# Performance work log

Hardware: AMD Instinct MI355X
Metric: run time of the kernel (lower is better)

The kernel has to match this reference:

```python
import jax, jax.numpy as jnp
import numpy as np

B, T, D, H = 32, 1024, 512, 512


def setup_inputs() -> dict:
    key = jax.random.key(0)
    ks = jax.random.split(key, 9)
    K = 1.0 / np.sqrt(H)
    u = lambda k, s: jax.random.uniform(k, s, jnp.float32, -K, K)
    return {
        "x": jax.random.normal(ks[0], (B, T, D), jnp.float32),
        "w_ih_fw": u(ks[1], (3 * H, D)),
        "w_hh_fw": u(ks[2], (3 * H, H)),
        "b_ih_fw": u(ks[3], (3 * H,)),
        "b_hh_fw": u(ks[4], (3 * H,)),
        "w_ih_bw": u(ks[5], (3 * H, D)),
        "w_hh_bw": u(ks[6], (3 * H, H)),
        "b_ih_bw": u(ks[7], (3 * H,)),
        "b_hh_bw": u(ks[8], (3 * H,)),
    }


def _gru_scan(x, w_ih, w_hh, b_ih, b_hh, reverse):
    # x: (B, T, D) -> precompute input projections for all steps: (T, B, 3H)
    b, t, d = x.shape
    h_dim = w_hh.shape[1]
    ih = jnp.einsum("btd,gd->tbg", x, w_ih) + b_ih

    def step(h, ih_t):
        hh = h @ w_hh.T + b_hh  # (B, 3H)
        r = jax.nn.sigmoid(ih_t[:, :h_dim] + hh[:, :h_dim])
        z = jax.nn.sigmoid(ih_t[:, h_dim:2 * h_dim] + hh[:, h_dim:2 * h_dim])
        n = jnp.tanh(ih_t[:, 2 * h_dim:] + r * hh[:, 2 * h_dim:])
        h_new = (1.0 - z) * n + z * h
        return h_new, h_new

    h0 = jnp.zeros((b, h_dim), x.dtype)
    h_last, ys = jax.lax.scan(step, h0, ih, reverse=reverse)
    # ys: (T, B, H), aligned to original time indices even when reverse=True
    return jnp.transpose(ys, (1, 0, 2)), h_last


def reference(x, w_ih_fw, w_hh_fw, b_ih_fw, b_hh_fw, w_ih_bw, w_hh_bw, b_ih_bw, b_hh_bw):
    out_fw, h_fw = _gru_scan(x, w_ih_fw, w_hh_fw, b_ih_fw, b_hh_fw, reverse=False)
    out_bw, h_bw = _gru_scan(x, w_ih_bw, w_hh_bw, b_ih_bw, b_hh_bw, reverse=True)
    outputs = jnp.concatenate([out_fw, out_bw], axis=-1)  # (B, T, 2H)
    return outputs, h_fw, h_bw
```

## Files before the change

kernel.cpp:

```cpp
#include <hip/hip_runtime.h>


#define T_LEN 1024
#define B_SZ  32
#define D_SZ  512
#define H_SZ  512
#define NWG_DIR 32
#define JW 16
#define NTHR 512

typedef __attribute__((ext_vector_type(8))) _Float16 half8;
typedef __attribute__((ext_vector_type(4))) float f32x4;
typedef __attribute__((ext_vector_type(4))) int int4v;

__device__ __forceinline__ _Float16 f2h(float f) { return (_Float16)f; }
__device__ __forceinline__ float sigm_f(float v) {
  return __builtin_amdgcn_rcpf(1.f + __expf(-v));
}
__device__ __forceinline__ float tanh_f(float v) {
  return 1.f - 2.f * __builtin_amdgcn_rcpf(1.f + __expf(2.f * v));
}
__device__ __forceinline__ void bar_lgkm() {
  asm volatile("s_waitcnt lgkmcnt(0)\ns_barrier" ::: "memory");
}

__global__ __launch_bounds__(NTHR, 2)
void gru2_persistent(const float* __restrict__ x,
                     const float* __restrict__ wih_fw, const float* __restrict__ whh_fw,
                     const float* __restrict__ bih_fw, const float* __restrict__ bhh_fw,
                     const float* __restrict__ wih_bw, const float* __restrict__ whh_bw,
                     const float* __restrict__ bih_bw, const float* __restrict__ bhh_bw,
                     float* __restrict__ out,
                     unsigned* __restrict__ hexu,
                     unsigned* __restrict__ flags)
{
  __shared__ float Cp[24 * 272];
  __shared__ float biasLds[96];

  const int bid  = blockIdx.x;
  const int dir  = bid >> 5;
  const int g    = bid & 31;
  const int tid  = threadIdx.x;
  const int wave = tid >> 6;
  const int lane = tid & 63;

  const float* wih = dir ? wih_bw : wih_fw;
  const float* whh = dir ? whh_bw : whh_fw;
  const float* bih = dir ? bih_bw : bih_fw;
  const float* bhh = dir ? bhh_bw : bhh_fw;

  if (tid < 48) {
    int grow = (tid >> 4) * H_SZ + g * JW + (tid & 15);
    biasLds[tid]      = bih[grow];
    biasLds[48 + tid] = bhh[grow];
  }

  const bool isHh = (wave >= 4);
  const int  wv   = wave & 3;
  const int  wm   = wv & 1;
  const int  kh   = wv >> 1;

  half8 Bf[3][8];
  {
    const float* W = isHh ? whh : wih;
    #pragma unroll
    for (int gam = 0; gam < 3; ++gam) {
      const int row = gam * H_SZ + g * JW + (lane & 15);
      #pragma unroll
      for (int i = 0; i < 8; ++i) {
        const float* src = W + (size_t)row * D_SZ + (kh * 8 + i) * 32 + ((lane >> 4) << 3);
        float4 v0 = *(const float4*)(src);
        float4 v1 = *(const float4*)(src + 4);
        half8 b;
        b[0]=f2h(v0.x); b[1]=f2h(v0.y); b[2]=f2h(v0.z); b[3]=f2h(v0.w);
        b[4]=f2h(v1.x); b[5]=f2h(v1.y); b[6]=f2h(v1.z); b[7]=f2h(v1.w);
        Bf[gam][i] = b;
      }
    }
  }

  const int arow = wm * 16 + (lane & 15);
  const int koff = (lane >> 4) << 3;
  const float* const xwavebase = x + (size_t)arow * T_LEN * D_SZ + kh * 256 + koff;

  float4 xn[16];
  if (!isHh) {
    const int t0 = dir ? (T_LEN - 1) : 0;
    const float* base = xwavebase + (size_t)t0 * D_SZ;
    #pragma unroll
    for (int i = 0; i < 8; ++i) {
      xn[2*i]   = *(const float4*)(base + i * 32);
      xn[2*i+1] = *(const float4*)(base + i * 32 + 4);
    }
  }
  __syncthreads();

  float hreg = 0.f;
  const int gb = tid >> 4;
  const int gj = tid & 15;
  float* hlast = out + (size_t)B_SZ * T_LEN * (2 * H_SZ) + (size_t)dir * B_SZ * H_SZ;
  const unsigned* const fa = flags + (size_t)dir * NWG_DIR + kh * 16 + (lane & 15);

  for (int s = 0; s < T_LEN; ++s) {
    const int t = dir ? (T_LEN - 1 - s) : s;
    const bool hasNext = (s + 1 < T_LEN);

    f32x4 acc[3] = {{0.f,0.f,0.f,0.f},{0.f,0.f,0.f,0.f},{0.f,0.f,0.f,0.f}};

    if (!isHh) {
      half8 a[8];
      #pragma unroll
      for (int i = 0; i < 8; ++i) {
        float4 u = xn[2*i], w = xn[2*i+1];
        half8 h;
        h[0]=f2h(u.x); h[1]=f2h(u.y); h[2]=f2h(u.z); h[3]=f2h(u.w);
        h[4]=f2h(w.x); h[5]=f2h(w.y); h[6]=f2h(w.z); h[7]=f2h(w.w);
        a[i] = h;
      }
      #pragma unroll
      for (int i = 0; i < 8; ++i)
        #pragma unroll
        for (int gam = 0; gam < 3; ++gam)
          acc[gam] = __builtin_amdgcn_mfma_f32_16x16x32_f16(a[i], Bf[gam][i], acc[gam], 0, 0, 0);
    } else if (s > 0) {
      {
        unsigned va, vb;
        asm volatile("global_load_dword %0, %1, off sc0 sc1" : "=&v"(va) : "v"(fa));
        asm volatile("global_load_dword %0, %1, off sc0 sc1" : "=&v"(vb) : "v"(fa));
        for (;;) {
          asm volatile("s_waitcnt vmcnt(1)" ::: "memory");
          if (__all(va >= (unsigned)s)) break;
          asm volatile("global_load_dword %0, %1, off sc0 sc1" : "=&v"(va) : "v"(fa));
          asm volatile("s_waitcnt vmcnt(1)" ::: "memory");
          if (__all(vb >= (unsigned)s)) break;
          asm volatile("global_load_dword %0, %1, off sc0 sc1" : "=&v"(vb) : "v"(fa));
        }
        asm volatile("s_waitcnt vmcnt(0)" ::: "memory");
      }
      const char* p0 = (const char*)hexu
          + (((size_t)dir * 2 + ((s - 1) & 1)) * (B_SZ * (H_SZ / 2))) * 4
          + (size_t)arow * (H_SZ * 2) + (size_t)(kh * 256 + koff) * 2;
      int4v hv[8];
      asm volatile(
        "global_load_dwordx4 %0, %8, off sc0 sc1\n\t"
        "global_load_dwordx4 %1, %8, off offset:64 sc0 sc1\n\t"
        "global_load_dwordx4 %2, %8, off offset:128 sc0 sc1\n\t"
        "global_load_dwordx4 %3, %8, off offset:192 sc0 sc1\n\t"
        "global_load_dwordx4 %4, %8, off offset:256 sc0 sc1\n\t"
        "global_load_dwordx4 %5, %8, off offset:320 sc0 sc1\n\t"
        "global_load_dwordx4 %6, %8, off offset:384 sc0 sc1\n\t"
        "global_load_dwordx4 %7, %8, off offset:448 sc0 sc1\n\t"
        "s_waitcnt vmcnt(0)"
        : "=&v"(hv[0]), "=&v"(hv[1]), "=&v"(hv[2]), "=&v"(hv[3]),
          "=&v"(hv[4]), "=&v"(hv[5]), "=&v"(hv[6]), "=&v"(hv[7])
        : "v"(p0) : "memory");
      __builtin_amdgcn_sched_barrier(0);
      #pragma unroll
      for (int i = 0; i < 8; ++i) {
        half8 a = __builtin_bit_cast(half8, hv[i]);
        #pragma unroll
        for (int gam = 0; gam < 3; ++gam)
          acc[gam] = __builtin_amdgcn_mfma_f32_16x16x32_f16(a, Bf[gam][i], acc[gam], 0, 0, 0);
      }
    }

    {
      const int src = isHh ? 1 : 0;
      #pragma unroll
      for (int gam = 0; gam < 3; ++gam) {
        float* cp = Cp + (size_t)(((src*2 + kh)*3 + gam)*2 + wm) * 272
                       + ((lane >> 4) << 2) * 17 + (lane & 15);
        #pragma unroll
        for (int vv2 = 0; vv2 < 4; ++vv2) cp[vv2 * 17] = acc[gam][vv2];
      }
    }
    bar_lgkm();

    float hnS;
    {
      const int mb = gb >> 4, rb = gb & 15;
      float sih[3], shh[3];
      #pragma unroll
      for (int gam = 0; gam < 3; ++gam) {
        float aih = 0.f, ahh = 0.f;
        #pragma unroll
        for (int q = 0; q < 2; ++q) {
          aih += Cp[(size_t)(((0*2+q)*3+gam)*2 + mb) * 272 + rb * 17 + gj];
          ahh += Cp[(size_t)(((1*2+q)*3+gam)*2 + mb) * 272 + rb * 17 + gj];
        }
        sih[gam] = aih + biasLds[gam * 16 + gj];
        shh[gam] = ahh + biasLds[48 + gam * 16 + gj];
      }
      const float r = sigm_f(sih[0] + shh[0]);
      const float z = sigm_f(sih[1] + shh[1]);
      const float n = tanh_f(sih[2] + r * shh[2]);
      const float hn = (1.f - z) * n + z * hreg;
      hreg = hn;
      hnS = hn;

      const float hother = __shfl_xor(hn, 1);
      if ((gj & 1) == 0) {
        union { unsigned u; _Float16 h[2]; } pr;
        pr.h[0] = f2h(hn); pr.h[1] = f2h(hother);
        unsigned* hp = hexu + ((size_t)dir * 2 + (s & 1)) * (B_SZ * (H_SZ / 2))
                     + (size_t)gb * (H_SZ / 2) + (g * JW + gj) / 2;
        __hip_atomic_store(hp, pr.u, __ATOMIC_RELAXED, __HIP_MEMORY_SCOPE_AGENT);
      }
    }
    asm volatile("s_waitcnt vmcnt(0)" ::: "memory");
    bar_lgkm();
    if (tid == 0)
      __hip_atomic_store((unsigned*)&flags[(size_t)dir * NWG_DIR + g],
                         (unsigned)(s + 1),
                         __ATOMIC_RELAXED, __HIP_MEMORY_SCOPE_AGENT);

    out[((size_t)gb * T_LEN + t) * (2 * H_SZ) + dir * H_SZ + g * JW + gj] = hnS;
    if (s == T_LEN - 1) hlast[gb * H_SZ + g * JW + gj] = hnS;
    if (!isHh && hasNext) {
      const int tn = dir ? (T_LEN - 2 - s) : (s + 1);
      const float* base = xwavebase + (size_t)tn * D_SZ;
      #pragma unroll
      for (int i = 0; i < 8; ++i) {
        xn[2*i]   = *(const float4*)(base + i * 32);
        xn[2*i+1] = *(const float4*)(base + i * 32 + 4);
      }
    }
  }
}

extern "C" void kernel_launch(void* const* d_in, const int* in_sizes, int n_in,
                              void* d_out, int out_size, void* d_ws, size_t ws_size,
                              hipStream_t stream) {
  const float* x      = (const float*)d_in[0];
  const float* wih_fw = (const float*)d_in[1];
  const float* whh_fw = (const float*)d_in[2];
  const float* bih_fw = (const float*)d_in[3];
  const float* bhh_fw = (const float*)d_in[4];
  const float* wih_bw = (const float*)d_in[5];
  const float* whh_bw = (const float*)d_in[6];
  const float* bih_bw = (const float*)d_in[7];
  const float* bhh_bw = (const float*)d_in[8];
  float* out = (float*)d_out;

  const size_t FLAGS_BYTES = 256;
  const size_t HEX_BYTES   = (size_t)2 * 2 * B_SZ * (H_SZ / 2) * sizeof(unsigned);
  if (ws_size < FLAGS_BYTES + HEX_BYTES) return;

  unsigned* flags = (unsigned*)d_ws;
  unsigned* hexu  = (unsigned*)((char*)d_ws + FLAGS_BYTES);

  hipMemsetAsync(flags, 0, FLAGS_BYTES, stream);
  gru2_persistent<<<dim3(64), dim3(NTHR), 0, stream>>>(
      x, wih_fw, whh_fw, bih_fw, bhh_fw, wih_bw, whh_bw, bih_bw, bhh_bw,
      out, hexu, flags);
}
```

Measured before the change: 4.414 ms.

## Co-locate each direction's workgroups on one XCD and use XCD-local coherence for exchange

The launch grows to 256 workgroups and keeps only those with blockIdx%8 in {0,1}, relying on round-robin XCD dispatch so each direction's 32 workgroups share one XCD. At startup every workgroup records its XCC id and checks that each direction is uniform and the two directions differ. If so, hidden-state exchange and flag polling use sc0-only loads and stores, which go through the shared L2 instead of bypassing to device-coherent memory. A grid-wide spin barrier and fallback paths guard against other placements, at the cost of extra startup synchronisation, more code, and reliance on undocumented dispatch order.

```diff
diff --git a/kernel.cpp b/kernel.cpp
--- a/kernel.cpp
+++ b/kernel.cpp
@@ -32,14 +32,19 @@
                      const float* __restrict__ bih_bw, const float* __restrict__ bhh_bw,
                      float* __restrict__ out,
                      unsigned* __restrict__ hexu,
-                     unsigned* __restrict__ flags)
+                     unsigned* __restrict__ flags,
+                     unsigned* __restrict__ xcdmap,
+                     unsigned* __restrict__ gbar)
 {
+  const int bid = blockIdx.x;
+  const int dir = bid & 7;
+  if (dir >= 2) return;
+  const int g = bid >> 3;
+
   __shared__ float Cp[24 * 272];
   __shared__ float biasLds[96];
-
-  const int bid  = blockIdx.x;
-  const int dir  = bid >> 5;
-  const int g    = bid & 31;
+  __shared__ int fastSh;
+
   const int tid  = threadIdx.x;
   const int wave = tid >> 6;
   const int lane = tid & 63;
@@ -54,6 +59,43 @@
     biasLds[tid]      = bih[grow];
     biasLds[48 + tid] = bhh[grow];
   }
+
+  {
+    unsigned xcc;
+    asm volatile("s_getreg_b32 %0, hwreg(20, 0, 32)" : "=s"(xcc));
+    if (tid == 0)
+      __hip_atomic_store(&xcdmap[dir * NWG_DIR + g], xcc + 1u,
+                         __ATOMIC_RELAXED, __HIP_MEMORY_SCOPE_AGENT);
+    if (wave == 0) {
+      unsigned v = 0u; int bud = 1 << 16; bool ok = true;
+      for (;;) {
+        v = __hip_atomic_load(&xcdmap[lane], __ATOMIC_RELAXED,
+                              __HIP_MEMORY_SCOPE_AGENT);
+        if (__all(v != 0u)) break;
+        if (--bud < 0) { ok = false; break; }
+        __builtin_amdgcn_s_sleep(8);
+      }
+      const unsigned ref0 = __shfl(v, 0);
+      const unsigned ref1 = __shfl(v, NWG_DIR);
+      const bool uni = __all((lane < NWG_DIR) ? (v == ref0) : (v == ref1));
+      if (lane == 0) fastSh = (ok && uni && ref0 != ref1) ? 1 : 0;
+    }
+  }
+  __syncthreads();
+  const bool fast = (fastSh != 0);
+  __builtin_amdgcn_fence(__ATOMIC_ACQUIRE, "agent");
+  __syncthreads();
+
+  if (tid == 0) {
+    __hip_atomic_fetch_add(gbar, 1u, __ATOMIC_RELAXED, __HIP_MEMORY_SCOPE_AGENT);
+    int bud = 1 << 20;
+    while (__hip_atomic_load(gbar, __ATOMIC_RELAXED,
+                             __HIP_MEMORY_SCOPE_AGENT) < 64u) {
+      if (--bud < 0) break;
+      __builtin_amdgcn_s_sleep(8);
+    }
+  }
+  __syncthreads();
 
   const bool isHh = (wave >= 4);
   const int  wv   = wave & 3;
@@ -100,6 +142,7 @@
   const int gj = tid & 15;
   float* hlast = out + (size_t)B_SZ * T_LEN * (2 * H_SZ) + (size_t)dir * B_SZ * H_SZ;
   const unsigned* const fa = flags + (size_t)dir * NWG_DIR + kh * 16 + (lane & 15);
+  int pollbud = 1 << 21;
 
   for (int s = 0; s < T_LEN; ++s) {
     const int t = dir ? (T_LEN - 1 - s) : s;
@@ -123,44 +166,79 @@
         for (int gam = 0; gam < 3; ++gam)
           acc[gam] = __builtin_amdgcn_mfma_f32_16x16x32_f16(a[i], Bf[gam][i], acc[gam], 0, 0, 0);
     } else if (s > 0) {
-      {
-        unsigned va, vb;
-        asm volatile("global_load_dword %0, %1, off sc0 sc1" : "=&v"(va) : "v"(fa));
-        asm volatile("global_load_dword %0, %1, off sc0 sc1" : "=&v"(vb) : "v"(fa));
+      if (fast) {
         for (;;) {
-          asm volatile("s_waitcnt vmcnt(1)" ::: "memory");
-          if (__all(va >= (unsigned)s)) break;
+          unsigned vv;
+          asm volatile("global_load_dword %0, %1, off sc0\ns_waitcnt vmcnt(0)"
+                       : "=&v"(vv) : "v"(fa) : "memory");
+          if (__all(vv >= (unsigned)s)) break;
+          if (--pollbud < 0) break;
+        }
+        const char* p0 = (const char*)hexu
+            + (((size_t)dir * 2 + ((s - 1) & 1)) * (B_SZ * (H_SZ / 2))) * 4
+            + (size_t)arow * (H_SZ * 2) + (size_t)(kh * 256 + koff) * 2;
+        int4v hv[8];
+        asm volatile(
+          "global_load_dwordx4 %0, %8, off sc0\n\t"
+          "global_load_dwordx4 %1, %8, off offset:64 sc0\n\t"
+          "global_load_dwordx4 %2, %8, off offset:128 sc0\n\t"
+          "global_load_dwordx4 %3, %8, off offset:192 sc0\n\t"
+          "global_load_dwordx4 %4, %8, off offset:256 sc0\n\t"
+          "global_load_dwordx4 %5, %8, off offset:320 sc0\n\t"
+          "global_load_dwordx4 %6, %8, off offset:384 sc0\n\t"
+          "global_load_dwordx4 %7, %8, off offset:448 sc0\n\t"
+          "s_waitcnt vmcnt(0)"
+          : "=&v"(hv[0]), "=&v"(hv[1]), "=&v"(hv[2]), "=&v"(hv[3]),
+            "=&v"(hv[4]), "=&v"(hv[5]), "=&v"(hv[6]), "=&v"(hv[7])
+          : "v"(p0) : "memory");
+        __builtin_amdgcn_sched_barrier(0);
+        #pragma unroll
+        for (int i = 0; i < 8; ++i) {
+          half8 a = __builtin_bit_cast(half8, hv[i]);
+          #pragma unroll
+          for (int gam = 0; gam < 3; ++gam)
+            acc[gam] = __builtin_amdgcn_mfma_f32_16x16x32_f16(a, Bf[gam][i], acc[gam], 0, 0, 0);
+        }
+      } else {
+        {
+          unsigned va, vb;
           asm volatile("global_load_dword %0, %1, off sc0 sc1" : "=&v"(va) : "v"(fa));
-          asm volatile("s_waitcnt vmcnt(1)" ::: "memory");
-          if (__all(vb >= (unsigned)s)) break;
           asm volatile("global_load_dword %0, %1, off sc0 sc1" : "=&v"(vb) : "v"(fa));
-        }
-        asm volatile("s_waitcnt vmcnt(0)" ::: "memory");
-      }
-      const char* p0 = (const char*)hexu
-          + (((size_t)dir * 2 + ((s - 1) & 1)) * (B_SZ * (H_SZ / 2))) * 4
-          + (size_t)arow * (H_SZ * 2) + (size_t)(kh * 256 + koff) * 2;
-      int4v hv[8];
-      asm volatile(
-        "global_load_dwordx4 %0, %8, off sc0 sc1\n\t"
-        "global_load_dwordx4 %1, %8, off offset:64 sc0 sc1\n\t"
-        "global_load_dwordx4 %2, %8, off offset:128 sc0 sc1\n\t"
-        "global_load_dwordx4 %3, %8, off offset:192 sc0 sc1\n\t"
-        "global_load_dwordx4 %4, %8, off offset:256 sc0 sc1\n\t"
-        "global_load_dwordx4 %5, %8, off offset:320 sc0 sc1\n\t"
-        "global_load_dwordx4 %6, %8, off offset:384 sc0 sc1\n\t"
-        "global_load_dwordx4 %7, %8, off offset:448 sc0 sc1\n\t"
-        "s_waitcnt vmcnt(0)"
-        : "=&v"(hv[0]), "=&v"(hv[1]), "=&v"(hv[2]), "=&v"(hv[3]),
-          "=&v"(hv[4]), "=&v"(hv[5]), "=&v"(hv[6]), "=&v"(hv[7])
-        : "v"(p0) : "memory");
-      __builtin_amdgcn_sched_barrier(0);
-      #pragma unroll
-      for (int i = 0; i < 8; ++i) {
-        half8 a = __builtin_bit_cast(half8, hv[i]);
-        #pragma unroll
-        for (int gam = 0; gam < 3; ++gam)
-          acc[gam] = __builtin_amdgcn_mfma_f32_16x16x32_f16(a, Bf[gam][i], acc[gam], 0, 0, 0);
+          for (;;) {
+            asm volatile("s_waitcnt vmcnt(1)" ::: "memory");
+            if (__all(va >= (unsigned)s)) break;
+            asm volatile("global_load_dword %0, %1, off sc0 sc1" : "=&v"(va) : "v"(fa));
+            asm volatile("s_waitcnt vmcnt(1)" ::: "memory");
+            if (__all(vb >= (unsigned)s)) break;
+            asm volatile("global_load_dword %0, %1, off sc0 sc1" : "=&v"(vb) : "v"(fa));
+          }
+          asm volatile("s_waitcnt vmcnt(0)" ::: "memory");
+        }
+        const char* p0 = (const char*)hexu
+            + (((size_t)dir * 2 + ((s - 1) & 1)) * (B_SZ * (H_SZ / 2))) * 4
+            + (size_t)arow * (H_SZ * 2) + (size_t)(kh * 256 + koff) * 2;
+        int4v hv[8];
+        asm volatile(
+          "global_load_dwordx4 %0, %8, off sc0 sc1\n\t"
+          "global_load_dwordx4 %1, %8, off offset:64 sc0 sc1\n\t"
+          "global_load_dwordx4 %2, %8, off offset:128 sc0 sc1\n\t"
+          "global_load_dwordx4 %3, %8, off offset:192 sc0 sc1\n\t"
+          "global_load_dwordx4 %4, %8, off offset:256 sc0 sc1\n\t"
+          "global_load_dwordx4 %5, %8, off offset:320 sc0 sc1\n\t"
+          "global_load_dwordx4 %6, %8, off offset:384 sc0 sc1\n\t"
+          "global_load_dwordx4 %7, %8, off offset:448 sc0 sc1\n\t"
+          "s_waitcnt vmcnt(0)"
+          : "=&v"(hv[0]), "=&v"(hv[1]), "=&v"(hv[2]), "=&v"(hv[3]),
+            "=&v"(hv[4]), "=&v"(hv[5]), "=&v"(hv[6]), "=&v"(hv[7])
+          : "v"(p0) : "memory");
+        __builtin_amdgcn_sched_barrier(0);
+        #pragma unroll
+        for (int i = 0; i < 8; ++i) {
+          half8 a = __builtin_bit_cast(half8, hv[i]);
+          #pragma unroll
+          for (int gam = 0; gam < 3; ++gam)
+            acc[gam] = __builtin_amdgcn_mfma_f32_16x16x32_f16(a, Bf[gam][i], acc[gam], 0, 0, 0);
+        }
       }
     }
 
@@ -204,15 +282,24 @@
         pr.h[0] = f2h(hn); pr.h[1] = f2h(hother);
         unsigned* hp = hexu + ((size_t)dir * 2 + (s & 1)) * (B_SZ * (H_SZ / 2))
                      + (size_t)gb * (H_SZ / 2) + (g * JW + gj) / 2;
-        __hip_atomic_store(hp, pr.u, __ATOMIC_RELAXED, __HIP_MEMORY_SCOPE_AGENT);
+        if (fast)
+          asm volatile("global_store_dword %0, %1, off sc0"
+                       :: "v"(hp), "v"(pr.u) : "memory");
+        else
+          __hip_atomic_store(hp, pr.u, __ATOMIC_RELAXED, __HIP_MEMORY_SCOPE_AGENT);
       }
     }
     asm volatile("s_waitcnt vmcnt(0)" ::: "memory");
     bar_lgkm();
-    if (tid == 0)
-      __hip_atomic_store((unsigned*)&flags[(size_t)dir * NWG_DIR + g],
-                         (unsigned)(s + 1),
-                         __ATOMIC_RELAXED, __HIP_MEMORY_SCOPE_AGENT);
+    if (tid == 0) {
+      unsigned* fp = flags + (size_t)dir * NWG_DIR + g;
+      const unsigned fv = (unsigned)(s + 1);
+      if (fast)
+        asm volatile("global_store_dword %0, %1, off sc0"
+                     :: "v"(fp), "v"(fv) : "memory");
+      else
+        __hip_atomic_store(fp, fv, __ATOMIC_RELAXED, __HIP_MEMORY_SCOPE_AGENT);
+    }
 
     out[((size_t)gb * T_LEN + t) * (2 * H_SZ) + dir * H_SZ + g * JW + gj] = hnS;
     if (s == T_LEN - 1) hlast[gb * H_SZ + g * JW + gj] = hnS;
@@ -226,6 +313,8 @@
       }
     }
   }
+
+  __builtin_amdgcn_fence(__ATOMIC_RELEASE, "agent");
 }
 
 extern "C" void kernel_launch(void* const* d_in, const int* in_sizes, int n_in,
@@ -242,15 +331,17 @@
   const float* bhh_bw = (const float*)d_in[8];
   float* out = (float*)d_out;
 
-  const size_t FLAGS_BYTES = 256;
-  const size_t HEX_BYTES   = (size_t)2 * 2 * B_SZ * (H_SZ / 2) * sizeof(unsigned);
-  if (ws_size < FLAGS_BYTES + HEX_BYTES) return;
-
-  unsigned* flags = (unsigned*)d_ws;
-  unsigned* hexu  = (unsigned*)((char*)d_ws + FLAGS_BYTES);
-
-  hipMemsetAsync(flags, 0, FLAGS_BYTES, stream);
-  gru2_persistent<<<dim3(64), dim3(NTHR), 0, stream>>>(
+  const size_t CTRL_BYTES = 1024;
+  const size_t HEX_BYTES  = (size_t)2 * 2 * B_SZ * (H_SZ / 2) * sizeof(unsigned);
+  if (ws_size < CTRL_BYTES + HEX_BYTES) return;
+
+  unsigned* xcdmap = (unsigned*)d_ws;
+  unsigned* flags  = (unsigned*)((char*)d_ws + 256);
+  unsigned* gbar   = (unsigned*)((char*)d_ws + 512);
+  unsigned* hexu   = (unsigned*)((char*)d_ws + CTRL_BYTES);
+
+  hipMemsetAsync(d_ws, 0, CTRL_BYTES, stream);
+  gru2_persistent<<<dim3(256), dim3(NTHR), 0, stream>>>(
       x, wih_fw, whh_fw, bih_fw, bhh_fw, wih_bw, whh_bw, bih_bw, bhh_bw,
-      out, hexu, flags);
-}
+      out, hexu, flags, xcdmap, gbar);
+}
```

Result: faster. 3.925 ms (-11.1%).
